# Kernel tuning notes

Hardware: AMD Instinct MI355X
Metric: run time of the kernel (lower is better)

The kernel has to match this reference:

```python
import jax, jax.numpy as jnp
import numpy as np

N = 100000      # nodes
E = 1600000     # edges
F = 128         # num_node_features
C = 64          # graph_hidden_channels
NH = 256        # nhid
NOUT = 128      # nout
L = 4           # n_layers (hidden GCN layers)
G = 512         # number of graphs in batch


def setup_inputs() -> dict:
    key = jax.random.key(0)
    ks = jax.random.split(key, 10)
    x = jax.random.normal(ks[0], (N, F), jnp.float32)
    edge_index = jax.random.randint(ks[1], (2, E), 0, N, dtype=jnp.int64)
    batch = jnp.sort(jax.random.randint(ks[2], (N,), 0, G, dtype=jnp.int64))

    def w(k, shape, fan_in):
        return jax.random.normal(k, shape, jnp.float32) / np.float32(np.sqrt(fan_in))

    W0 = w(ks[3], (F, C), F)
    b0 = jnp.zeros((C,), jnp.float32)
    Wh = w(ks[4], (L, C, C), C)      # stacked hidden GCN weights
    bh = jnp.zeros((L, C), jnp.float32)
    W1 = w(ks[5], (C, NH), C)
    b1 = jnp.zeros((NH,), jnp.float32)
    W2 = w(ks[6], (NH, NOUT), NH)
    b2 = jnp.zeros((NOUT,), jnp.float32)
    return dict(x=x, edge_index=edge_index, batch=batch,
                W0=W0, b0=b0, Wh=Wh, bh=bh, W1=W1, b1=b1, W2=W2, b2=b2)


def _gcn_conv(h_in, W, b, src, dst, dinv):
    # PyG GCNConv: out_i = sum_{j->i} dinv_j * dinv_i * (x_j W) + dinv_i^2 * (x_i W) + b
    h = h_in @ W                                   # [N, C]
    coef = (dinv[src] * dinv[dst])[:, None]        # [E, 1]
    agg = jax.ops.segment_sum(h[src] * coef, dst, num_segments=N)
    agg = agg + h * (dinv * dinv)[:, None]         # self-loop term
    return agg + b


def reference(x, edge_index, batch, W0, b0, Wh, bh, W1, b1, W2, b2):
    src, dst = edge_index[0], edge_index[1]
    # degree with self loops (edge weight 1)
    deg = jax.ops.segment_sum(jnp.ones((E,), x.dtype), dst, num_segments=N) + 1.0
    dinv = jax.lax.rsqrt(deg)                      # [N]

    h = jax.nn.relu(_gcn_conv(x, W0, b0, src, dst, dinv))
    for i in range(L):
        h = jax.nn.relu(_gcn_conv(h, Wh[i], bh[i], src, dst, dinv))

    # global mean pool over graphs
    counts = jax.ops.segment_sum(jnp.ones((N,), x.dtype), batch, num_segments=G)
    pooled = jax.ops.segment_sum(h, batch, num_segments=G) / jnp.maximum(counts, 1.0)[:, None]

    out = jax.nn.relu(pooled @ W1 + b1)
    out = out @ W2 + b2
    return out
```

## Files before the change

### kernel.cpp

```cpp
#include <hip/hip_runtime.h>
#include <hip/hip_fp16.h>
#include <stddef.h>

static constexpr int Nn    = 100000;
static constexpr int Ee    = 1600000;
static constexpr int Ff    = 128;
static constexpr int Cc    = 64;
static constexpr int NHh   = 256;
static constexpr int NOUTt = 128;
static constexpr int Ll    = 4;
static constexpr int Gg    = 512;

static constexpr int SCAN_BLK = 1024;
static constexpr int NBLK_SCAN = (Nn + SCAN_BLK - 1) / SCAN_BLK;

static constexpr int NSUB   = (Nn + 511) / 512;
static constexpr int SUBCAP = 10240;

__global__ __launch_bounds__(256) void bin_kernel(const int* __restrict__ src,
                                                  const int* __restrict__ dst,
                                                  int* __restrict__ sb,
                                                  int* __restrict__ scnt, int E) {
    __shared__ int lcnt[NSUB], lbase[NSUB];
    const int tid = threadIdx.x;
    for (int i = tid; i < NSUB; i += 256) lcnt[i] = 0;
    __syncthreads();
    const int base = blockIdx.x * 2048;
    int pk[8], ps[8], lr[8];
    #pragma unroll
    for (int i = 0; i < 8; ++i) {
        int e = base + i * 256 + tid;
        if (e < E) {
            int d = dst[e], s = src[e];
            int sub = d >> 9;
            ps[i] = sub;
            pk[i] = s | ((d & 511) << 17);
            lr[i] = atomicAdd(&lcnt[sub], 1);
        } else ps[i] = -1;
    }
    __syncthreads();
    for (int i = tid; i < NSUB; i += 256) lbase[i] = atomicAdd(&scnt[i], lcnt[i]);
    __syncthreads();
    #pragma unroll
    for (int i = 0; i < 8; ++i) {
        if (ps[i] >= 0) {
            int pos = lbase[ps[i]] + lr[i];
            if (pos < SUBCAP) sb[(size_t)ps[i] * SUBCAP + pos] = pk[i];
        }
    }
}

__global__ __launch_bounds__(512) void cnt3_kernel(const int* __restrict__ sb,
                                                   const int* __restrict__ scnt,
                                                   int* __restrict__ cnt) {
    __shared__ int lcnt[512];
    const int sub = blockIdx.x, tid = threadIdx.x;
    lcnt[tid] = 0;
    __syncthreads();
    const int n = scnt[sub];
    const int* bp = sb + (size_t)sub * SUBCAP;
    for (int i = tid; i < n; i += 512) atomicAdd(&lcnt[(bp[i] >> 17) & 511], 1);
    __syncthreads();
    int node = sub * 512 + tid;
    if (node < Nn) cnt[node] = lcnt[tid];
}

__global__ void dinv_kernel(const int* __restrict__ cnt, float* __restrict__ dinv, int n) {
    int i = blockIdx.x * blockDim.x + threadIdx.x;
    if (i < n) dinv[i] = rsqrtf((float)cnt[i] + 1.0f);
}

__global__ __launch_bounds__(SCAN_BLK) void scan1_kernel(const int* __restrict__ cnt,
                                                         int* __restrict__ row_off,
                                                         int* __restrict__ bsum, int n) {
    __shared__ int sd[SCAN_BLK];
    int tid = threadIdx.x;
    int gid = blockIdx.x * SCAN_BLK + tid;
    int v = (gid < n) ? cnt[gid] : 0;
    sd[tid] = v;
    __syncthreads();
    #pragma unroll
    for (int off = 1; off < SCAN_BLK; off <<= 1) {
        int t = (tid >= off) ? sd[tid - off] : 0;
        __syncthreads();
        sd[tid] += t;
        __syncthreads();
    }
    if (gid < n) row_off[gid + 1] = sd[tid];
    if (tid == SCAN_BLK - 1) bsum[blockIdx.x] = sd[tid];
}

__global__ __launch_bounds__(128) void scan2_kernel(const int* __restrict__ bsum,
                                                    int* __restrict__ boff, int nb) {
    __shared__ int sd[128];
    int tid = threadIdx.x;
    sd[tid] = (tid < nb) ? bsum[tid] : 0;
    __syncthreads();
    #pragma unroll
    for (int off = 1; off < 128; off <<= 1) {
        int t = (tid >= off) ? sd[tid - off] : 0;
        __syncthreads();
        sd[tid] += t;
        __syncthreads();
    }
    if (tid < nb) boff[tid] = (tid == 0) ? 0 : sd[tid - 1];
}

__global__ void scan3_kernel(int* __restrict__ row_off, const int* __restrict__ boff, int n) {
    int gid = blockIdx.x * blockDim.x + threadIdx.x;
    if (gid < n) row_off[gid + 1] += boff[gid >> 10];
    if (gid == 0) row_off[0] = 0;
}

__global__ __launch_bounds__(512) void fill3_kernel(const int* __restrict__ sb,
                                                    const int* __restrict__ scnt,
                                                    const int* __restrict__ roff,
                                                    int* __restrict__ csr) {
    __shared__ int lcnt[512], lofs[512];
    __shared__ int gbase;
    const int sub = blockIdx.x, tid = threadIdx.x;
    lcnt[tid] = 0;
    if (tid == 0) gbase = roff[sub * 512];
    __syncthreads();
    const int n = scnt[sub];
    const int* bp = sb + (size_t)sub * SUBCAP;
    for (int i = tid; i < n; i += 512) atomicAdd(&lcnt[(bp[i] >> 17) & 511], 1);
    __syncthreads();
    int v = lcnt[tid];
    lofs[tid] = v;
    __syncthreads();
    #pragma unroll
    for (int off = 1; off < 512; off <<= 1) {
        int t = (tid >= off) ? lofs[tid - off] : 0;
        __syncthreads();
        lofs[tid] += t;
        __syncthreads();
    }
    int excl = lofs[tid] - v;
    __syncthreads();
    lcnt[tid] = excl;
    __syncthreads();
    for (int i = tid; i < n; i += 512) {
        int e = bp[i];
        int pos = atomicAdd(&lcnt[(e >> 17) & 511], 1);
        csr[gbase + pos] = e & 0x1FFFF;
    }
}

__device__ inline float4 h4_to_f4(float2 raw) {
    __half2 a = *reinterpret_cast<__half2*>(&raw.x);
    __half2 b = *reinterpret_cast<__half2*>(&raw.y);
    float2 fa = __half22float2(a), fb = __half22float2(b);
    return make_float4(fa.x, fa.y, fb.x, fb.y);
}

template<int CIN>
__global__ __launch_bounds__(256) void gemm_xw(const float* __restrict__ X,
                                               const float* __restrict__ W,
                                               const float* __restrict__ dinv,
                                               __half* __restrict__ Y, int n) {
    __shared__ float hs[64][68];
    __shared__ float ws[64][64];
    const int tid = threadIdx.x;
    const int tx  = tid & 15;
    const int ty  = tid >> 4;
    const int rowbase = blockIdx.x * 64;

    float acc[4][4] = {};

    for (int k0 = 0; k0 < CIN; k0 += 64) {
        #pragma unroll
        for (int i = 0; i < 4; ++i) {
            int r = ty + i * 16;
            int gr = rowbase + r;
            float4 v = make_float4(0.f, 0.f, 0.f, 0.f);
            if (gr < n) v = *(const float4*)(X + (size_t)gr * CIN + k0 + tx * 4);
            *(float4*)&hs[r][tx * 4] = v;
        }
        #pragma unroll
        for (int i = 0; i < 4; ++i) {
            int k = ty + i * 16;
            *(float4*)&ws[k][tx * 4] = *(const float4*)(W + (size_t)(k0 + k) * 64 + tx * 4);
        }
        __syncthreads();

        #pragma unroll 4
        for (int k = 0; k < 64; ++k) {
            float4 w = *(const float4*)&ws[k][tx * 4];
            float h0 = hs[ty * 4 + 0][k];
            float h1 = hs[ty * 4 + 1][k];
            float h2 = hs[ty * 4 + 2][k];
            float h3 = hs[ty * 4 + 3][k];
            acc[0][0] += h0 * w.x; acc[0][1] += h0 * w.y; acc[0][2] += h0 * w.z; acc[0][3] += h0 * w.w;
            acc[1][0] += h1 * w.x; acc[1][1] += h1 * w.y; acc[1][2] += h1 * w.z; acc[1][3] += h1 * w.w;
            acc[2][0] += h2 * w.x; acc[2][1] += h2 * w.y; acc[2][2] += h2 * w.z; acc[2][3] += h2 * w.w;
            acc[3][0] += h3 * w.x; acc[3][1] += h3 * w.y; acc[3][2] += h3 * w.z; acc[3][3] += h3 * w.w;
        }
        __syncthreads();
    }

    #pragma unroll
    for (int i = 0; i < 4; ++i) {
        int gr = rowbase + ty * 4 + i;
        if (gr < n) {
            float di = dinv[gr];
            __half2 p0 = __floats2half2_rn(acc[i][0] * di, acc[i][1] * di);
            __half2 p1 = __floats2half2_rn(acc[i][2] * di, acc[i][3] * di);
            float2 st;
            *reinterpret_cast<__half2*>(&st.x) = p0;
            *reinterpret_cast<__half2*>(&st.y) = p1;
            *reinterpret_cast<float2*>(Y + (size_t)gr * 64 + tx * 4) = st;
        }
    }
}

__global__ __launch_bounds__(256) void gather_agg(const int* __restrict__ row_off,
                                                  const int* __restrict__ csr_src,
                                                  const float* __restrict__ dinv,
                                                  const __half* __restrict__ t,
                                                  const float* __restrict__ b,
                                                  float* __restrict__ out, int n) {
    const int lane = threadIdx.x & 63;
    const int node = (blockIdx.x * blockDim.x + threadIdx.x) >> 6;
    if (node >= n) return;
    const int sub = lane >> 4;
    const int c4  = lane & 15;

    const int base = row_off[node];
    const int end  = row_off[node + 1];

    float4 acc = make_float4(0.f, 0.f, 0.f, 0.f);

    for (int k0 = base; k0 < end; k0 += 64) {
        int myidx = (k0 + lane < end) ? csr_src[k0 + lane] : 0;
        int nk = min(64, end - k0);
        int k = 0;
        for (; k + 8 <= nk; k += 8) {
            int s0 = __shfl(myidx, k + sub);
            int s1 = __shfl(myidx, k + 4 + sub);
            float2 r0 = *(const float2*)(t + (size_t)s0 * 64 + c4 * 4);
            float2 r1 = *(const float2*)(t + (size_t)s1 * 64 + c4 * 4);
            float4 v0 = h4_to_f4(r0);
            float4 v1 = h4_to_f4(r1);
            acc.x += v0.x; acc.y += v0.y; acc.z += v0.z; acc.w += v0.w;
            acc.x += v1.x; acc.y += v1.y; acc.z += v1.z; acc.w += v1.w;
        }
        for (; k < nk; k += 4) {
            int kk = k + sub;
            int s = __shfl(myidx, kk);
            if (kk < nk) {
                float4 v = h4_to_f4(*(const float2*)(t + (size_t)s * 64 + c4 * 4));
                acc.x += v.x; acc.y += v.y; acc.z += v.z; acc.w += v.w;
            }
        }
    }

    #pragma unroll
    for (int off = 16; off < 64; off <<= 1) {
        acc.x += __shfl_xor(acc.x, off);
        acc.y += __shfl_xor(acc.y, off);
        acc.z += __shfl_xor(acc.z, off);
        acc.w += __shfl_xor(acc.w, off);
    }

    if (sub == 0) {
        float di = dinv[node];
        float4 self = h4_to_f4(*(const float2*)(t + (size_t)node * 64 + c4 * 4));
        float4 bb   = *(const float4*)(b + c4 * 4);
        float4 r;
        r.x = fmaxf(di * (acc.x + self.x) + bb.x, 0.f);
        r.y = fmaxf(di * (acc.y + self.y) + bb.y, 0.f);
        r.z = fmaxf(di * (acc.z + self.z) + bb.z, 0.f);
        r.w = fmaxf(di * (acc.w + self.w) + bb.w, 0.f);
        *(float4*)(out + (size_t)node * 64 + c4 * 4) = r;
    }
}

__global__ void gbounds_kernel(const int* __restrict__ batch, int* __restrict__ gstart, int n) {
    int i = blockIdx.x * blockDim.x + threadIdx.x;
    if (i >= n) return;
    int bi = batch[i];
    int bp = (i == 0) ? -1 : batch[i - 1];
    for (int g = bp + 1; g <= bi; ++g) gstart[g] = i;
    if (i == n - 1) {
        for (int g = bi + 1; g <= Gg; ++g) gstart[g] = n;
    }
}

__global__ __launch_bounds__(256) void pool_graph(const float* __restrict__ h,
                                                  const int* __restrict__ gstart,
                                                  float* __restrict__ pooled) {
    __shared__ float sd[4][64];
    const int g    = blockIdx.x;
    const int lane = threadIdx.x & 63;
    const int wv   = threadIdx.x >> 6;
    const int s = gstart[g], e = gstart[g + 1];
    float acc = 0.f;
    for (int i = s + wv; i < e; i += 4) acc += h[(size_t)i * 64 + lane];
    sd[wv][lane] = acc;
    __syncthreads();
    if (wv == 0) {
        float sum = sd[0][lane] + sd[1][lane] + sd[2][lane] + sd[3][lane];
        float c = (float)(e - s);
        pooled[(size_t)g * 64 + lane] = sum / fmaxf(c, 1.f);
    }
}

__global__ void mlp1_kernel(const float* __restrict__ P, const float* __restrict__ W1,
                            const float* __restrict__ b1, float* __restrict__ H) {
    int gid = blockIdx.x * blockDim.x + threadIdx.x;
    if (gid >= Gg * NHh) return;
    int j = gid & (NHh - 1), g = gid >> 8;
    const float* p = P + (size_t)g * Cc;
    float s = b1[j];
    #pragma unroll 8
    for (int k = 0; k < Cc; ++k) s += p[k] * W1[(size_t)k * NHh + j];
    H[gid] = fmaxf(s, 0.f);
}

__global__ void mlp2_kernel(const float* __restrict__ H, const float* __restrict__ W2,
                            const float* __restrict__ b2, float* __restrict__ O) {
    int gid = blockIdx.x * blockDim.x + threadIdx.x;
    if (gid >= Gg * NOUTt) return;
    int j = gid & (NOUTt - 1), g = gid >> 7;
    const float* h = H + (size_t)g * NHh;
    float s = b2[j];
    #pragma unroll 8
    for (int k = 0; k < NHh; ++k) s += h[k] * W2[(size_t)k * NOUTt + j];
    O[gid] = s;
}

extern "C" void kernel_launch(void* const* d_in, const int* in_sizes, int n_in,
                              void* d_out, int out_size, void* d_ws, size_t ws_size,
                              hipStream_t stream) {
    const float* x     = (const float*)d_in[0];
    const int*   ei    = (const int*)  d_in[1];
    const int*   batch = (const int*)  d_in[2];
    const float* W0    = (const float*)d_in[3];
    const float* b0    = (const float*)d_in[4];
    const float* Wh    = (const float*)d_in[5];
    const float* bh    = (const float*)d_in[6];
    const float* W1    = (const float*)d_in[7];
    const float* b1    = (const float*)d_in[8];
    const float* W2    = (const float*)d_in[9];
    const float* b2    = (const float*)d_in[10];

    const int* src = ei;
    const int* dst = ei + Ee;

    char* ws = (char*)d_ws;
    constexpr size_t OFF_DINV  = 0;
    constexpr size_t OFF_CNT   = 400384;
    constexpr size_t OFF_ROFF  = OFF_CNT + 400384;
    constexpr size_t OFF_BSUM  = OFF_ROFF + 400384;
    constexpr size_t OFF_BOFF  = OFF_BSUM + 1024;
    constexpr size_t OFF_SCNT  = OFF_BOFF + 1024;
    constexpr size_t OFF_CSR   = OFF_SCNT + 1024;
    constexpr size_t OFF_T     = OFF_CSR + 6400256;
    constexpr size_t OFF_A     = OFF_T + 12800256;
    constexpr size_t OFF_POOL  = OFF_A + (size_t)Nn * 64 * 4;
    constexpr size_t OFF_GST   = OFF_POOL + (size_t)Gg * Cc * 4;
    constexpr size_t OFF_HID   = OFF_GST + 4096;
    const size_t OFF_SB = OFF_T;

    float*  dinv   = (float*) (ws + OFF_DINV);
    int*    cnt    = (int*)   (ws + OFF_CNT);
    int*    roff   = (int*)   (ws + OFF_ROFF);
    int*    bsum   = (int*)   (ws + OFF_BSUM);
    int*    boff   = (int*)   (ws + OFF_BOFF);
    int*    scnt   = (int*)   (ws + OFF_SCNT);
    int*    csrs   = (int*)   (ws + OFF_CSR);
    int*    sb     = (int*)   (ws + OFF_SB);
    __half* T      = (__half*)(ws + OFF_T);
    float*  A      = (float*) (ws + OFF_A);
    float*  pooled = (float*) (ws + OFF_POOL);
    int*    gstart = (int*)   (ws + OFF_GST);
    float*  hid    = (float*) (ws + OFF_HID);

    hipMemsetAsync(scnt, 0, 1024, stream);
    bin_kernel<<<(Ee + 2047) / 2048, 256, 0, stream>>>(src, dst, sb, scnt, Ee);
    cnt3_kernel<<<NSUB, 512, 0, stream>>>(sb, scnt, cnt);
    dinv_kernel<<<(Nn + 255) / 256, 256, 0, stream>>>(cnt, dinv, Nn);
    scan1_kernel<<<NBLK_SCAN, SCAN_BLK, 0, stream>>>(cnt, roff, bsum, Nn);
    scan2_kernel<<<1, 128, 0, stream>>>(bsum, boff, NBLK_SCAN);
    scan3_kernel<<<(Nn + 255) / 256, 256, 0, stream>>>(roff, boff, Nn);
    fill3_kernel<<<NSUB, 512, 0, stream>>>(sb, scnt, roff, csrs);

    gbounds_kernel<<<(Nn + 255) / 256, 256, 0, stream>>>(batch, gstart, Nn);

    const int gemm_blocks = (Nn + 63) / 64;
    const int agg_blocks  = (Nn * 64 + 255) / 256;

    gemm_xw<128><<<gemm_blocks, 256, 0, stream>>>(x, W0, dinv, T, Nn);
    gather_agg<<<agg_blocks, 256, 0, stream>>>(roff, csrs, dinv, T, b0, A, Nn);

    for (int i = 0; i < Ll; ++i) {
        gemm_xw<64><<<gemm_blocks, 256, 0, stream>>>(A, Wh + (size_t)i * Cc * Cc, dinv, T, Nn);
        gather_agg<<<agg_blocks, 256, 0, stream>>>(roff, csrs, dinv, T, bh + (size_t)i * Cc, A, Nn);
    }

    pool_graph<<<Gg, 256, 0, stream>>>(A, gstart, pooled);

    mlp1_kernel<<<(Gg * NHh + 255) / 256, 256, 0, stream>>>(pooled, W1, b1, hid);
    mlp2_kernel<<<(Gg * NOUTt + 255) / 256, 256, 0, stream>>>(hid, W2, b2, (float*)d_out);
}
```

Measured before the change: 408.1 us.

## Store intermediate activations in fp16 and widen gather loads to 16 bytes

The aggregated hidden activations A are now stored as fp16 instead of fp32, so the GEMM, gather and pooling kernels read and write half as many bytes for them. A dedicated fp16-input GEMM converts rows to float in shared memory. The gather kernel now uses 8 lanes per row with 16-byte loads, processing 8 neighbors per pass instead of 4, which cuts shuffle and reduction work per edge. In exchange, activations are rounded to fp16 one more time per layer, adding precision loss.

```diff
diff --git a/kernel.cpp b/kernel.cpp
--- a/kernel.cpp
+++ b/kernel.cpp
@@ -147,18 +147,29 @@
     }
 }
 
-__device__ inline float4 h4_to_f4(float2 raw) {
-    __half2 a = *reinterpret_cast<__half2*>(&raw.x);
-    __half2 b = *reinterpret_cast<__half2*>(&raw.y);
-    float2 fa = __half22float2(a), fb = __half22float2(b);
-    return make_float4(fa.x, fa.y, fb.x, fb.y);
-}
-
-template<int CIN>
-__global__ __launch_bounds__(256) void gemm_xw(const float* __restrict__ X,
-                                               const float* __restrict__ W,
-                                               const float* __restrict__ dinv,
-                                               __half* __restrict__ Y, int n) {
+__device__ inline void add_h8(float acc[8], float4 raw) {
+    const __half2* hp = reinterpret_cast<const __half2*>(&raw);
+    #pragma unroll
+    for (int j = 0; j < 4; ++j) {
+        float2 f = __half22float2(hp[j]);
+        acc[2 * j]     += f.x;
+        acc[2 * j + 1] += f.y;
+    }
+}
+
+__device__ inline void cvt_h8(float4 raw, float v[8]) {
+    const __half2* hp = reinterpret_cast<const __half2*>(&raw);
+    #pragma unroll
+    for (int j = 0; j < 4; ++j) {
+        float2 f = __half22float2(hp[j]);
+        v[2 * j] = f.x; v[2 * j + 1] = f.y;
+    }
+}
+
+__global__ __launch_bounds__(256) void gemm_xw_f32(const float* __restrict__ X,
+                                                   const float* __restrict__ W,
+                                                   const float* __restrict__ dinv,
+                                                   __half* __restrict__ Y, int n) {
     __shared__ float hs[64][68];
     __shared__ float ws[64][64];
     const int tid = threadIdx.x;
@@ -168,13 +179,13 @@
 
     float acc[4][4] = {};
 
-    for (int k0 = 0; k0 < CIN; k0 += 64) {
+    for (int k0 = 0; k0 < Ff; k0 += 64) {
         #pragma unroll
         for (int i = 0; i < 4; ++i) {
             int r = ty + i * 16;
             int gr = rowbase + r;
             float4 v = make_float4(0.f, 0.f, 0.f, 0.f);
-            if (gr < n) v = *(const float4*)(X + (size_t)gr * CIN + k0 + tx * 4);
+            if (gr < n) v = *(const float4*)(X + (size_t)gr * Ff + k0 + tx * 4);
             *(float4*)&hs[r][tx * 4] = v;
         }
         #pragma unroll
@@ -214,65 +225,128 @@
     }
 }
 
+__global__ __launch_bounds__(256) void gemm_xw_f16(const __half* __restrict__ X,
+                                                   const float* __restrict__ W,
+                                                   const float* __restrict__ dinv,
+                                                   __half* __restrict__ Y, int n) {
+    __shared__ float hs[64][68];
+    __shared__ float ws[64][64];
+    const int tid = threadIdx.x;
+    const int tx  = tid & 15;
+    const int ty  = tid >> 4;
+    const int rowbase = blockIdx.x * 64;
+
+    float acc[4][4] = {};
+
+    #pragma unroll
+    for (int i = 0; i < 4; ++i) {
+        int r = ty + i * 16;
+        int gr = rowbase + r;
+        float4 v = make_float4(0.f, 0.f, 0.f, 0.f);
+        if (gr < n) {
+            float2 raw = *(const float2*)(X + (size_t)gr * 64 + tx * 4);
+            __half2 a = *reinterpret_cast<__half2*>(&raw.x);
+            __half2 b = *reinterpret_cast<__half2*>(&raw.y);
+            float2 fa = __half22float2(a), fb = __half22float2(b);
+            v = make_float4(fa.x, fa.y, fb.x, fb.y);
+        }
+        *(float4*)&hs[r][tx * 4] = v;
+    }
+    #pragma unroll
+    for (int i = 0; i < 4; ++i) {
+        int k = ty + i * 16;
+        *(float4*)&ws[k][tx * 4] = *(const float4*)(W + (size_t)k * 64 + tx * 4);
+    }
+    __syncthreads();
+
+    #pragma unroll 4
+    for (int k = 0; k < 64; ++k) {
+        float4 w = *(const float4*)&ws[k][tx * 4];
+        float h0 = hs[ty * 4 + 0][k];
+        float h1 = hs[ty * 4 + 1][k];
+        float h2 = hs[ty * 4 + 2][k];
+        float h3 = hs[ty * 4 + 3][k];
+        acc[0][0] += h0 * w.x; acc[0][1] += h0 * w.y; acc[0][2] += h0 * w.z; acc[0][3] += h0 * w.w;
+        acc[1][0] += h1 * w.x; acc[1][1] += h1 * w.y; acc[1][2] += h1 * w.z; acc[1][3] += h1 * w.w;
+        acc[2][0] += h2 * w.x; acc[2][1] += h2 * w.y; acc[2][2] += h2 * w.z; acc[2][3] += h2 * w.w;
+        acc[3][0] += h3 * w.x; acc[3][1] += h3 * w.y; acc[3][2] += h3 * w.z; acc[3][3] += h3 * w.w;
+    }
+
+    #pragma unroll
+    for (int i = 0; i < 4; ++i) {
+        int gr = rowbase + ty * 4 + i;
+        if (gr < n) {
+            float di = dinv[gr];
+            __half2 p0 = __floats2half2_rn(acc[i][0] * di, acc[i][1] * di);
+            __half2 p1 = __floats2half2_rn(acc[i][2] * di, acc[i][3] * di);
+            float2 st;
+            *reinterpret_cast<__half2*>(&st.x) = p0;
+            *reinterpret_cast<__half2*>(&st.y) = p1;
+            *reinterpret_cast<float2*>(Y + (size_t)gr * 64 + tx * 4) = st;
+        }
+    }
+}
+
 __global__ __launch_bounds__(256) void gather_agg(const int* __restrict__ row_off,
                                                   const int* __restrict__ csr_src,
                                                   const float* __restrict__ dinv,
                                                   const __half* __restrict__ t,
                                                   const float* __restrict__ b,
-                                                  float* __restrict__ out, int n) {
+                                                  __half* __restrict__ out, int n) {
     const int lane = threadIdx.x & 63;
     const int node = (blockIdx.x * blockDim.x + threadIdx.x) >> 6;
     if (node >= n) return;
-    const int sub = lane >> 4;
-    const int c4  = lane & 15;
+    const int sub = lane >> 3;
+    const int c8  = lane & 7;
 
     const int base = row_off[node];
     const int end  = row_off[node + 1];
 
-    float4 acc = make_float4(0.f, 0.f, 0.f, 0.f);
+    float acc[8] = {};
 
     for (int k0 = base; k0 < end; k0 += 64) {
         int myidx = (k0 + lane < end) ? csr_src[k0 + lane] : 0;
         int nk = min(64, end - k0);
         int k = 0;
-        for (; k + 8 <= nk; k += 8) {
+        for (; k + 16 <= nk; k += 16) {
             int s0 = __shfl(myidx, k + sub);
-            int s1 = __shfl(myidx, k + 4 + sub);
-            float2 r0 = *(const float2*)(t + (size_t)s0 * 64 + c4 * 4);
-            float2 r1 = *(const float2*)(t + (size_t)s1 * 64 + c4 * 4);
-            float4 v0 = h4_to_f4(r0);
-            float4 v1 = h4_to_f4(r1);
-            acc.x += v0.x; acc.y += v0.y; acc.z += v0.z; acc.w += v0.w;
-            acc.x += v1.x; acc.y += v1.y; acc.z += v1.z; acc.w += v1.w;
-        }
-        for (; k < nk; k += 4) {
+            int s1 = __shfl(myidx, k + 8 + sub);
+            float4 r0 = *(const float4*)(t + (size_t)s0 * 64 + c8 * 8);
+            float4 r1 = *(const float4*)(t + (size_t)s1 * 64 + c8 * 8);
+            add_h8(acc, r0);
+            add_h8(acc, r1);
+        }
+        for (; k < nk; k += 8) {
             int kk = k + sub;
             int s = __shfl(myidx, kk);
             if (kk < nk) {
-                float4 v = h4_to_f4(*(const float2*)(t + (size_t)s * 64 + c4 * 4));
-                acc.x += v.x; acc.y += v.y; acc.z += v.z; acc.w += v.w;
+                float4 r = *(const float4*)(t + (size_t)s * 64 + c8 * 8);
+                add_h8(acc, r);
             }
         }
     }
 
     #pragma unroll
-    for (int off = 16; off < 64; off <<= 1) {
-        acc.x += __shfl_xor(acc.x, off);
-        acc.y += __shfl_xor(acc.y, off);
-        acc.z += __shfl_xor(acc.z, off);
-        acc.w += __shfl_xor(acc.w, off);
+    for (int off = 8; off < 64; off <<= 1) {
+        #pragma unroll
+        for (int j = 0; j < 8; ++j) acc[j] += __shfl_xor(acc[j], off);
     }
 
     if (sub == 0) {
         float di = dinv[node];
-        float4 self = h4_to_f4(*(const float2*)(t + (size_t)node * 64 + c4 * 4));
-        float4 bb   = *(const float4*)(b + c4 * 4);
-        float4 r;
-        r.x = fmaxf(di * (acc.x + self.x) + bb.x, 0.f);
-        r.y = fmaxf(di * (acc.y + self.y) + bb.y, 0.f);
-        r.z = fmaxf(di * (acc.z + self.z) + bb.z, 0.f);
-        r.w = fmaxf(di * (acc.w + self.w) + bb.w, 0.f);
-        *(float4*)(out + (size_t)node * 64 + c4 * 4) = r;
+        float selfv[8];
+        cvt_h8(*(const float4*)(t + (size_t)node * 64 + c8 * 8), selfv);
+        float4 b0 = *(const float4*)(b + c8 * 8);
+        float4 b1 = *(const float4*)(b + c8 * 8 + 4);
+        float bb[8] = {b0.x, b0.y, b0.z, b0.w, b1.x, b1.y, b1.z, b1.w};
+        __half2 o[4];
+        #pragma unroll
+        for (int j = 0; j < 4; ++j) {
+            float v0 = fmaxf(di * (acc[2 * j]     + selfv[2 * j])     + bb[2 * j],     0.f);
+            float v1 = fmaxf(di * (acc[2 * j + 1] + selfv[2 * j + 1]) + bb[2 * j + 1], 0.f);
+            o[j] = __floats2half2_rn(v0, v1);
+        }
+        *(float4*)(out + (size_t)node * 64 + c8 * 8) = *reinterpret_cast<float4*>(o);
     }
 }
 
@@ -287,7 +361,7 @@
     }
 }
 
-__global__ __launch_bounds__(256) void pool_graph(const float* __restrict__ h,
+__global__ __launch_bounds__(256) void pool_graph(const __half* __restrict__ h,
                                                   const int* __restrict__ gstart,
                                                   float* __restrict__ pooled) {
     __shared__ float sd[4][64];
@@ -296,7 +370,7 @@
     const int wv   = threadIdx.x >> 6;
     const int s = gstart[g], e = gstart[g + 1];
     float acc = 0.f;
-    for (int i = s + wv; i < e; i += 4) acc += h[(size_t)i * 64 + lane];
+    for (int i = s + wv; i < e; i += 4) acc += __half2float(h[(size_t)i * 64 + lane]);
     sd[wv][lane] = acc;
     __syncthreads();
     if (wv == 0) {
@@ -358,7 +432,7 @@
     constexpr size_t OFF_CSR   = OFF_SCNT + 1024;
     constexpr size_t OFF_T     = OFF_CSR + 6400256;
     constexpr size_t OFF_A     = OFF_T + 12800256;
-    constexpr size_t OFF_POOL  = OFF_A + (size_t)Nn * 64 * 4;
+    constexpr size_t OFF_POOL  = OFF_A + 12800256;
     constexpr size_t OFF_GST   = OFF_POOL + (size_t)Gg * Cc * 4;
     constexpr size_t OFF_HID   = OFF_GST + 4096;
     const size_t OFF_SB = OFF_T;
@@ -372,7 +446,7 @@
     int*    csrs   = (int*)   (ws + OFF_CSR);
     int*    sb     = (int*)   (ws + OFF_SB);
     __half* T      = (__half*)(ws + OFF_T);
-    float*  A      = (float*) (ws + OFF_A);
+    __half* A      = (__half*)(ws + OFF_A);
     float*  pooled = (float*) (ws + OFF_POOL);
     int*    gstart = (int*)   (ws + OFF_GST);
     float*  hid    = (float*) (ws + OFF_HID);
@@ -391,11 +465,11 @@
     const int gemm_blocks = (Nn + 63) / 64;
     const int agg_blocks  = (Nn * 64 + 255) / 256;
 
-    gemm_xw<128><<<gemm_blocks, 256, 0, stream>>>(x, W0, dinv, T, Nn);
+    gemm_xw_f32<<<gemm_blocks, 256, 0, stream>>>(x, W0, dinv, T, Nn);
     gather_agg<<<agg_blocks, 256, 0, stream>>>(roff, csrs, dinv, T, b0, A, Nn);
 
     for (int i = 0; i < Ll; ++i) {
-        gemm_xw<64><<<gemm_blocks, 256, 0, stream>>>(A, Wh + (size_t)i * Cc * Cc, dinv, T, Nn);
+        gemm_xw_f16<<<gemm_blocks, 256, 0, stream>>>(A, Wh + (size_t)i * Cc * Cc, dinv, T, Nn);
         gather_agg<<<agg_blocks, 256, 0, stream>>>(roff, csrs, dinv, T, bh + (size_t)i * Cc, A, Nn);
     }
 
```

Result: no change. 406.8 us (-0.3%).
